# Kernel tuning notes

Measured on AMD Instinct MI355X. Metric: run time of the kernel, lower is better.

## Reference

```python
import jax, jax.numpy as jnp
import numpy as np

B, S, HID = 2, 2048, 2048
H, HKV, D = 16, 4, 128

def _rope(x, cos, sin):
    # x: [B,h,S,D]; cos/sin: [1,1,S,D//2]
    d = x.shape[-1] // 2
    x1, x2 = x[..., :d], x[..., d:]
    y1 = x1 * cos + x2 * sin
    y2 = -x1 * sin + x2 * cos
    return jnp.concatenate([y1, y2], axis=-1)

def _rmsnorm(x):
    eps = jnp.finfo(x.dtype).eps
    return x * jax.lax.rsqrt(jnp.mean(jnp.square(x), axis=-1, keepdims=True) + eps)

def setup_inputs() -> dict:
    key = jax.random.key(0)
    ks = jax.random.split(key, 5)
    x = jax.random.normal(ks[0], (B, S, HID), dtype=jnp.float32)
    # realistic rotary tables
    half = D // 2
    inv_freq = 1.0 / (10000.0 ** (jnp.arange(half, dtype=jnp.float32) / half))
    t = jnp.arange(S, dtype=jnp.float32)
    freqs = t[:, None] * inv_freq[None, :]            # [S, D//2]
    cos = jnp.cos(freqs)[None, None]                  # [1,1,S,D//2]
    sin = jnp.sin(freqs)[None, None]
    s = 0.02
    Wq = jax.random.normal(ks[1], (H * D, HID), dtype=jnp.float32) * s
    Wk = jax.random.normal(ks[2], (HKV * D, HID), dtype=jnp.float32) * s
    Wv = jax.random.normal(ks[3], (HKV * D, HID), dtype=jnp.float32) * s
    Wo = jax.random.normal(ks[4], (HID, H * D), dtype=jnp.float32) * s
    return {"x": x, "cos": cos, "sin": sin, "Wq": Wq, "Wk": Wk, "Wv": Wv, "Wo": Wo}

def reference(x, cos, sin, Wq, Wk, Wv, Wo):
    b, s, _ = x.shape
    rep = H // HKV
    q = (x @ Wq.T).reshape(b, s, H, D).transpose(0, 2, 1, 3)      # [B,H,S,D]
    k = (x @ Wk.T).reshape(b, s, HKV, D).transpose(0, 2, 1, 3)    # [B,Hkv,S,D]
    v = (x @ Wv.T).reshape(b, s, HKV, D).transpose(0, 2, 1, 3)
    k = jnp.repeat(k, rep, axis=1)                                # GQA expand
    v = jnp.repeat(v, rep, axis=1)
    q = _rmsnorm(_rope(q, cos, sin))
    k = _rmsnorm(_rope(k, cos, sin))
    scores = jnp.einsum('bhqd,bhkd->bhqk', q, k) * (D ** -0.5)
    causal = jnp.tril(jnp.ones((s, s), dtype=bool))
    scores = jnp.where(causal, scores, -jnp.inf)
    attn = jax.nn.softmax(scores, axis=-1)
    out = jnp.einsum('bhqk,bhkd->bhqd', attn, v)                  # [B,H,S,D]
    out = out.transpose(0, 2, 1, 3).reshape(b, s, H * D)
    return out @ Wo.T
```

## Files before the change

kernel.cpp:

```cpp
#include <hip/hip_runtime.h>
#include <hip/hip_bf16.h>

#define B_  2
#define S_  2048
#define HID_ 2048
#define H_  16
#define HKV_ 4
#define D_  128

typedef __bf16 bf16_t;
typedef bf16_t bf16x8 __attribute__((ext_vector_type(8)));
typedef float f32x4 __attribute__((ext_vector_type(4)));

typedef __attribute__((address_space(3))) unsigned int lds_u32_t;
typedef const __attribute__((address_space(1))) unsigned int glob_u32_t;

__device__ __forceinline__ void gl2lds16(const bf16_t* g, bf16_t* l) {
    __builtin_amdgcn_global_load_lds((glob_u32_t*)g, (lds_u32_t*)l, 16, 0, 0);
}

__device__ __forceinline__ unsigned packbf2(float a, float b) {
    union { bf16_t h[2]; unsigned u; } p;
    p.h[0] = (bf16_t)a;
    p.h[1] = (bf16_t)b;
    return p.u;
}

__global__ void detect_dtype(const unsigned* __restrict__ x, int* __restrict__ flag) {
    int lane = threadIdx.x;
    int c = 0;
#pragma unroll
    for (int i = 0; i < 16; ++i) {
        unsigned w = x[lane * 16 + i];
        unsigned e = (w >> 7) & 0xFF;
        c += (e >= 117 && e <= 137) ? 1 : 0;
    }
#pragma unroll
    for (int m = 1; m < 64; m <<= 1) c += __shfl_xor(c, m, 64);
    if (lane == 0) *flag = (c >= 512) ? 1 : 0;
}

struct Cseg { const void* src; bf16_t* dst; int n8; };

__global__ __launch_bounds__(256) void convert_bf16(Cseg s0, Cseg s1, Cseg s2, Cseg s3,
                                                    const int* __restrict__ flagp) {
    Cseg s = (blockIdx.y == 0) ? s0 : (blockIdx.y == 1) ? s1 : (blockIdx.y == 2) ? s2 : s3;
    const int i = blockIdx.x * 256 + threadIdx.x;
    if (i >= s.n8) return;
    if (*flagp) {
        ((uint4*)s.dst)[i] = ((const uint4*)s.src)[i];
    } else {
        const float4* p = (const float4*)s.src + (size_t)i * 2;
        float4 u = p[0], v = p[1];
        bf16x8 r;
        r[0] = (bf16_t)u.x; r[1] = (bf16_t)u.y; r[2] = (bf16_t)u.z; r[3] = (bf16_t)u.w;
        r[4] = (bf16_t)v.x; r[5] = (bf16_t)v.y; r[6] = (bf16_t)v.z; r[7] = (bf16_t)v.w;
        *(bf16x8*)(s.dst + (size_t)i * 8) = r;
    }
}

__global__ __launch_bounds__(256) void gemm_lds(const bf16_t* __restrict__ A,
                                                const bf16_t* __restrict__ W,
                                                void* __restrict__ C,
                                                int M, int N, int K,
                                                const int* __restrict__ flagp, int osel) {
    __shared__ bf16_t As[128 * 32];
    __shared__ bf16_t Bs[128 * 32];

    const int tid = threadIdx.x;
    const int w = tid >> 6;
    const int lane = tid & 63;
    const int r = lane & 15;
    const int quad = lane >> 4;
    const int m0 = blockIdx.y * 128;
    const int n0 = blockIdx.x * 128;
    const bool of32 = osel && (*flagp == 0);

    const int mh = (w & 1) * 64;
    const int nh = (w >> 1) * 64;

    const int c0 = w * 2;
    const int srow = lane >> 2;
    const int scol = (lane & 3) * 8;
    const bf16_t* Ag0 = A + (size_t)(m0 + c0 * 16 + srow) * K + scol;
    const bf16_t* Ag1 = A + (size_t)(m0 + c0 * 16 + 16 + srow) * K + scol;
    const bf16_t* Wg0 = W + (size_t)(n0 + c0 * 16 + srow) * K + scol;
    const bf16_t* Wg1 = W + (size_t)(n0 + c0 * 16 + 16 + srow) * K + scol;
    bf16_t* Al0 = As + c0 * 512;
    bf16_t* Al1 = As + (c0 + 1) * 512;
    bf16_t* Bl0 = Bs + c0 * 512;
    bf16_t* Bl1 = Bs + (c0 + 1) * 512;

    f32x4 acc[4][4] = {};

    for (int k0 = 0; k0 < K; k0 += 32) {
        __syncthreads();
        gl2lds16(Ag0 + k0, Al0);
        gl2lds16(Ag1 + k0, Al1);
        gl2lds16(Wg0 + k0, Bl0);
        gl2lds16(Wg1 + k0, Bl1);
        __syncthreads();

        bf16x8 a[4], b[4];
#pragma unroll
        for (int mi = 0; mi < 4; ++mi)
            a[mi] = *(const bf16x8*)&As[(mh + mi * 16 + r) * 32 + quad * 8];
#pragma unroll
        for (int ni = 0; ni < 4; ++ni)
            b[ni] = *(const bf16x8*)&Bs[(nh + ni * 16 + r) * 32 + quad * 8];
#pragma unroll
        for (int mi = 0; mi < 4; ++mi)
#pragma unroll
            for (int ni = 0; ni < 4; ++ni)
                acc[mi][ni] = __builtin_amdgcn_mfma_f32_16x16x32_bf16(a[mi], b[ni], acc[mi][ni], 0, 0, 0);
    }

#pragma unroll
    for (int mi = 0; mi < 4; ++mi) {
#pragma unroll
        for (int ni = 0; ni < 4; ++ni) {
#pragma unroll
            for (int g = 0; g < 4; ++g) {
                const int row = m0 + mh + mi * 16 + quad * 4 + g;
                const int col = n0 + nh + ni * 16 + r;
                if (of32) ((float*)C)[(size_t)row * N + col] = acc[mi][ni][g];
                else ((__hip_bfloat16*)C)[(size_t)row * N + col] = __float2bfloat16(acc[mi][ni][g]);
            }
        }
    }
}

template <bool F32>
__device__ __forceinline__ bf16x8 load8(const void* base, size_t off) {
    bf16x8 r;
    if constexpr (F32) {
        const float4* p = (const float4*)((const float*)base + off);
        float4 u = p[0], v = p[1];
        r[0] = (bf16_t)u.x; r[1] = (bf16_t)u.y; r[2] = (bf16_t)u.z; r[3] = (bf16_t)u.w;
        r[4] = (bf16_t)v.x; r[5] = (bf16_t)v.y; r[6] = (bf16_t)v.z; r[7] = (bf16_t)v.w;
    } else {
        r = *(const bf16x8*)((const bf16_t*)base + off);
    }
    return r;
}

template <bool AF32, bool WF32, bool OF32>
__device__ __forceinline__ void gemm_body(const void* __restrict__ A, const void* __restrict__ W,
                                          void* __restrict__ C, int M, int N, int K) {
    const int wave = threadIdx.x >> 6;
    const int lane = threadIdx.x & 63;
    const int r = lane & 15;
    const int quad = lane >> 4;
    const int m0 = blockIdx.y * 64 + wave * 16;
    const int n0 = blockIdx.x * 64;

    f32x4 acc[4] = {};
    const size_t aoff = (size_t)(m0 + r) * K + quad * 8;
    const size_t woff = (size_t)(n0 + r) * K + quad * 8;

    for (int k0 = 0; k0 < K; k0 += 32) {
        bf16x8 a = load8<AF32>(A, aoff + k0);
#pragma unroll
        for (int ns = 0; ns < 4; ++ns) {
            bf16x8 b = load8<WF32>(W, woff + (size_t)(ns * 16) * K + k0);
            acc[ns] = __builtin_amdgcn_mfma_f32_16x16x32_bf16(a, b, acc[ns], 0, 0, 0);
        }
    }

#pragma unroll
    for (int ns = 0; ns < 4; ++ns) {
#pragma unroll
        for (int reg = 0; reg < 4; ++reg) {
            int m = m0 + quad * 4 + reg;
            int n = n0 + ns * 16 + r;
            if constexpr (OF32) ((float*)C)[(size_t)m * N + n] = acc[ns][reg];
            else ((__hip_bfloat16*)C)[(size_t)m * N + n] = __float2bfloat16(acc[ns][reg]);
        }
    }
}

__global__ __launch_bounds__(256) void gemm_bt(const void* __restrict__ A, const void* __restrict__ W,
                                               void* __restrict__ C, int M, int N, int K,
                                               const int* __restrict__ flagp, int mode) {
    const int bf = *flagp;
    if (bf) {
        gemm_body<false, false, false>(A, W, C, M, N, K);
    } else if (mode == 0) {
        gemm_body<true, true, false>(A, W, C, M, N, K);
    } else {
        gemm_body<false, true, true>(A, W, C, M, N, K);
    }
}

__global__ __launch_bounds__(256) void rope_rms(__hip_bfloat16* __restrict__ qk,
                                                const void* __restrict__ cosp,
                                                const void* __restrict__ sinp,
                                                int NH, int ld, const int* __restrict__ flagp) {
    const int bf = *flagp;
    const int wave = threadIdx.x >> 6;
    const int lane = threadIdx.x & 63;
    const int row = blockIdx.x * 4 + wave;
    const int h = row % NH;
    const int bs = row / NH;
    const int s = bs % S_;

    __hip_bfloat16* p = qk + (size_t)bs * ld + h * D_;
    float x1 = __bfloat162float(p[lane]);
    float x2 = __bfloat162float(p[lane + 64]);
    float c, sn, eps;
    if (bf) {
        c   = __bfloat162float(((const __hip_bfloat16*)cosp)[s * 64 + lane]);
        sn  = __bfloat162float(((const __hip_bfloat16*)sinp)[s * 64 + lane]);
        eps = 0.0078125f;
    } else {
        c   = ((const float*)cosp)[s * 64 + lane];
        sn  = ((const float*)sinp)[s * 64 + lane];
        eps = 1.1920929e-07f;
    }
    float y1 = x1 * c + x2 * sn;
    float y2 = x2 * c - x1 * sn;
    float ss = y1 * y1 + y2 * y2;
#pragma unroll
    for (int m = 1; m < 64; m <<= 1) ss += __shfl_xor(ss, m, 64);
    float rinv = rsqrtf(ss * (1.0f / 128.0f) + eps);
    p[lane]      = __float2bfloat16(y1 * rinv);
    p[lane + 64] = __float2bfloat16(y2 * rinv);
}

__global__ __launch_bounds__(256) void post_qkv(__hip_bfloat16* __restrict__ qkv,
                                                const void* __restrict__ cosp,
                                                const void* __restrict__ sinp,
                                                bf16_t* __restrict__ Kp,
                                                unsigned* __restrict__ Vp,
                                                const void* __restrict__ WoS,
                                                bf16_t* __restrict__ WoD,
                                                const int* __restrict__ flagp) {
    const int bx = blockIdx.x;
    const int y = blockIdx.y;
    const int tid = threadIdx.x;

    if (y <= 1) {
        if (y == 1 && bx >= 4096) return;
        const int bf = *flagp;
        const int wave = tid >> 6;
        const int lane = tid & 63;
        const int row = bx * 4 + wave;
        const int h  = (y == 0) ? (row & 15) : (row & 3);
        const int bs = (y == 0) ? (row >> 4) : (row >> 2);
        const int s = bs & 2047;

        __hip_bfloat16* p = qkv + (size_t)bs * 3072 + (y ? 2048 : 0) + h * D_;
        float x1 = __bfloat162float(p[lane]);
        float x2 = __bfloat162float(p[lane + 64]);
        float c, sn, eps;
        if (bf) {
            c   = __bfloat162float(((const __hip_bfloat16*)cosp)[s * 64 + lane]);
            sn  = __bfloat162float(((const __hip_bfloat16*)sinp)[s * 64 + lane]);
            eps = 0.0078125f;
        } else {
            c   = ((const float*)cosp)[s * 64 + lane];
            sn  = ((const float*)sinp)[s * 64 + lane];
            eps = 1.1920929e-07f;
        }
        float y1 = x1 * c + x2 * sn;
        float y2 = x2 * c - x1 * sn;
        float ss = y1 * y1 + y2 * y2;
#pragma unroll
        for (int m = 1; m < 64; m <<= 1) ss += __shfl_xor(ss, m, 64);
        float rinv = rsqrtf(ss * (1.0f / 128.0f) + eps);
        const float y1r = y1 * rinv, y2r = y2 * rinv;
        if (y == 0) {
            p[lane]      = __float2bfloat16(y1r);
            p[lane + 64] = __float2bfloat16(y2r);
        } else {
            const int b = bs >> 11;
            const int kt = s >> 5;
            const int r32 = s & 31;
            const int gy = b * 4 + h;
            bf16_t* base = Kp + ((size_t)(gy * 64 + kt) * 32 + r32) * 128;
            const int sw = r32 & 15;
            base[(((lane >> 3) ^ sw) << 3) + (lane & 7)]       = (bf16_t)y1r;
            base[(((8 + (lane >> 3)) ^ sw) << 3) + (lane & 7)] = (bf16_t)y2r;
        }
    } else if (y == 2) {
        if (bx >= 4096) return;
        const int idx = bx * 256 + tid;
        const int j  = idx & 3;
        const int sl = (idx >> 2) & 3;
        const int d  = (idx >> 4) & 127;
        const int kt = (idx >> 11) & 63;
        const int gy = idx >> 17;
        const int s2 = sl ^ ((d >> 1) & 3);
        const int kp = s2 * 4 + j;
        const int kvh = gy & 3;
        const int b = gy >> 2;
        const unsigned short* p = (const unsigned short*)qkv
            + (size_t)(b * S_ + 32 * kt + kp) * 3072 + 2560 + kvh * D_ + d;
        unsigned lo = p[0];
        unsigned hi = p[(size_t)16 * 3072];
        Vp[idx] = lo | (hi << 16);
    } else {
        if (bx >= 2048) return;
        const int i = bx * 256 + tid;
        if (*flagp) {
            ((uint4*)WoD)[i] = ((const uint4*)WoS)[i];
        } else {
            const float4* p4 = (const float4*)WoS + (size_t)i * 2;
            float4 u = p4[0], v = p4[1];
            bf16x8 rr;
            rr[0] = (bf16_t)u.x; rr[1] = (bf16_t)u.y; rr[2] = (bf16_t)u.z; rr[3] = (bf16_t)u.w;
            rr[4] = (bf16_t)v.x; rr[5] = (bf16_t)v.y; rr[6] = (bf16_t)v.z; rr[7] = (bf16_t)v.w;
            *(bf16x8*)(WoD + (size_t)i * 8) = rr;
        }
    }
}

#define M0F 16.5f

__global__ __launch_bounds__(512, 1) void attn_flash10(const __hip_bfloat16* __restrict__ Q,
                                                       const bf16_t* __restrict__ Kp,
                                                       const unsigned* __restrict__ Vp,
                                                       __hip_bfloat16* __restrict__ O) {
    __shared__ bf16_t   Kl[8][4096];
    __shared__ unsigned Vl[8][2048];
    __shared__ unsigned PbS[8][2][16][16];

    const int tid = threadIdx.x;
    const int w = tid >> 6;
    const int lane = tid & 63;
    const int r = lane & 15;
    const int quad = lane >> 4;

    const int id = blockIdx.x;
    const int gy = id & 7;
    const int u = id >> 3;
    const int hh = u & 3;
    const int i = u >> 2;
    const int kvh = gy & 3;
    const int b = gy >> 2;
    const int h = kvh * 4 + hh;

    const int s4 = w & 3;
    int tlo = (s4 == 0) ? i : (s4 == 1) ? (31 - i) : (s4 == 2) ? (16 + i) : (15 - i);
    const int qt = (w < 4) ? tlo : (63 - tlo);
    const int q0 = qt * 32;

    const bf16_t* Ksrc = Kp + (size_t)gy * (64 * 4096);
    const unsigned* Vsrc = Vp + (size_t)gy * (64 * 2048);
    bf16_t* klds = &Kl[w][0];
    unsigned* vlds = &Vl[w][0];

    bf16x8 qf[2][4];
#pragma unroll
    for (int t = 0; t < 2; ++t) {
        const bf16_t* qp = (const bf16_t*)Q + (size_t)(b * S_ + q0 + t * 16 + r) * 3072 + h * D_ + quad * 8;
#pragma unroll
        for (int c = 0; c < 4; ++c) qf[t][c] = *(const bf16x8*)(qp + c * 32);
    }

    f32x4 oacc[2][8] = {};
    f32x4 lacc[2] = {};

    bf16x8 ones;
#pragma unroll
    for (int j = 0; j < 8; ++j) ones[j] = (bf16_t)1.0f;

    const float SC2 = 0.08838834764831845f * 1.4426950408889634f;

    unsigned* pbw = &PbS[w][0][0][0];
    const int pwi = (((r >> 2) ^ quad) & 3) * 4 + (r & 3);
    const int pgrp = ((quad ^ (r >> 2)) & 3) * 4;
    const int vsw = (quad ^ ((r >> 1) & 3)) * 4;

#define ISSUEK(KT) do {                                                       \
        const bf16_t* ks_ = Ksrc + (size_t)(KT) * 4096 + lane * 8;            \
        _Pragma("unroll")                                                     \
        for (int jj = 0; jj < 8; ++jj) gl2lds16(ks_ + jj * 512, klds + jj * 512); \
    } while (0)
#define ISSUEV(KT) do {                                                       \
        const bf16_t* vs_ = (const bf16_t*)(Vsrc + (size_t)(KT) * 2048) + lane * 8; \
        _Pragma("unroll")                                                     \
        for (int jj = 0; jj < 8; ++jj) gl2lds16(vs_ + jj * 512, (bf16_t*)vlds + jj * 512); \
    } while (0)

    ISSUEK(0);
    ISSUEV(0);
    for (int kt = 0; kt <= qt; ++kt) {
        asm volatile("s_waitcnt vmcnt(8)" ::: "memory");

        bf16x8 kf[8];
#pragma unroll
        for (int c = 0; c < 4; ++c) {
            const int sA = ((quad + 4 * c) ^ r) * 8;
            kf[2 * c]     = *(const bf16x8*)&klds[r * 128 + sA];
            kf[2 * c + 1] = *(const bf16x8*)&klds[(16 + r) * 128 + sA];
        }
        asm volatile("s_waitcnt lgkmcnt(0)" ::: "memory");
        __builtin_amdgcn_sched_barrier(0);
        if (kt < qt) ISSUEK(kt + 1);
        __builtin_amdgcn_sched_barrier(0);

        f32x4 s0_[2] = {}, s1_[2] = {};
        __builtin_amdgcn_s_setprio(1);
#pragma unroll
        for (int c = 0; c < 4; ++c) {
#pragma unroll
            for (int t = 0; t < 2; ++t) {
                s0_[t] = __builtin_amdgcn_mfma_f32_16x16x32_bf16(qf[t][c], kf[2 * c], s0_[t], 0, 0, 0);
                s1_[t] = __builtin_amdgcn_mfma_f32_16x16x32_bf16(qf[t][c], kf[2 * c + 1], s1_[t], 0, 0, 0);
            }
        }
        __builtin_amdgcn_s_setprio(0);

        if (kt == qt) {
#pragma unroll
            for (int t = 0; t < 2; ++t)
#pragma unroll
                for (int g = 0; g < 4; ++g) {
                    const int qrow = q0 + t * 16 + quad * 4 + g;
                    if (kt * 32 + r > qrow)      s0_[t][g] = -1e38f;
                    if (kt * 32 + 16 + r > qrow) s1_[t][g] = -1e38f;
                }
        }

#pragma unroll
        for (int t = 0; t < 2; ++t)
#pragma unroll
            for (int g = 0; g < 4; ++g) {
                const float p0 = exp2f(fmaf(s0_[t][g], SC2, -M0F));
                const float p1 = exp2f(fmaf(s1_[t][g], SC2, -M0F));
                pbw[t * 256 + (quad * 4 + g) * 16 + pwi] = packbf2(p0, p1);
            }

        bf16x8 pf0 = *(const bf16x8*)&pbw[r * 16 + pgrp];
        bf16x8 pf1 = *(const bf16x8*)&pbw[256 + r * 16 + pgrp];

        lacc[0] = __builtin_amdgcn_mfma_f32_16x16x32_bf16(pf0, ones, lacc[0], 0, 0, 0);
        lacc[1] = __builtin_amdgcn_mfma_f32_16x16x32_bf16(pf1, ones, lacc[1], 0, 0, 0);

        if (kt < qt) asm volatile("s_waitcnt vmcnt(8)" ::: "memory");
        else         asm volatile("s_waitcnt vmcnt(0)" ::: "memory");

        bf16x8 vf[8];
#pragma unroll
        for (int ns = 0; ns < 8; ++ns)
            vf[ns] = *(const bf16x8*)&vlds[(ns * 16 + r) * 16 + vsw];
        asm volatile("s_waitcnt lgkmcnt(0)" ::: "memory");
        __builtin_amdgcn_sched_barrier(0);
        if (kt < qt) ISSUEV(kt + 1);
        __builtin_amdgcn_sched_barrier(0);

        __builtin_amdgcn_s_setprio(1);
#pragma unroll
        for (int ns = 0; ns < 8; ++ns) {
            oacc[0][ns] = __builtin_amdgcn_mfma_f32_16x16x32_bf16(pf0, vf[ns], oacc[0][ns], 0, 0, 0);
            oacc[1][ns] = __builtin_amdgcn_mfma_f32_16x16x32_bf16(pf1, vf[ns], oacc[1][ns], 0, 0, 0);
        }
        __builtin_amdgcn_s_setprio(0);
    }
#undef ISSUEK
#undef ISSUEV

#pragma unroll
    for (int t = 0; t < 2; ++t) {
#pragma unroll
        for (int g = 0; g < 4; ++g) {
            const float inv = 1.0f / lacc[t][g];
            const int qrow = q0 + t * 16 + quad * 4 + g;
            __hip_bfloat16* op = O + (size_t)(b * S_ + qrow) * 2048 + h * D_;
#pragma unroll
            for (int ns = 0; ns < 8; ++ns)
                op[ns * 16 + r] = __float2bfloat16(oacc[t][ns][g] * inv);
        }
    }
}

#define KT_ 32
#define LDK 136

__global__ __launch_bounds__(256, 2) void attn_flash3(const __hip_bfloat16* __restrict__ Q,
                                                      const __hip_bfloat16* __restrict__ K,
                                                      const __hip_bfloat16* __restrict__ V,
                                                      __hip_bfloat16* __restrict__ O,
                                                      int ldq, int ldkv, int ldo) {
    __shared__ unsigned short Ks[KT_][LDK];
    __shared__ unsigned int Vt[D_ * 16];
    __shared__ unsigned int Pb[4][2][16][16];

    const int tid = threadIdx.x;
    const int w = tid >> 6;
    const int lane = tid & 63;
    const int r = lane & 15;
    const int quad = lane >> 4;

    const int gy = blockIdx.y;
    const int kvh = gy % HKV_;
    const int b = gy / HKV_;
    const int qt = b ? blockIdx.x : (gridDim.x - 1 - blockIdx.x);
    const int q0 = qt * 32;
    const int h = kvh * 4 + w;

    bf16x8 qf[2][4];
#pragma unroll
    for (int t = 0; t < 2; ++t) {
        const bf16_t* qp = (const bf16_t*)Q + (size_t)(b * S_ + q0 + t * 16 + r) * ldq + h * D_ + quad * 8;
#pragma unroll
        for (int c = 0; c < 4; ++c) qf[t][c] = *(const bf16x8*)(qp + c * 32);
    }

    f32x4 oacc[2][8] = {};
    f32x4 lacc[2] = {};
    float m_i[2][4];
#pragma unroll
    for (int t = 0; t < 2; ++t)
#pragma unroll
        for (int g = 0; g < 4; ++g) m_i[t][g] = -3e38f;

    const bf16_t* Kg = (const bf16_t*)K + (size_t)b * S_ * ldkv + kvh * D_;
    const bf16_t* Vg = (const bf16_t*)V + (size_t)b * S_ * ldkv + kvh * D_;

    bf16x8 ones;
#pragma unroll
    for (int j = 0; j < 8; ++j) ones[j] = (bf16_t)1.0f;

    const float SC2 = 0.08838834764831845f * 1.4426950408889634f;

    const int skey = tid >> 4;
    const int sdc = tid & 15;
    union U4 { uint4 u; unsigned short s[8]; };
    U4 rk0, rk1, rv0, rv1;
    {
        const size_t o0 = (size_t)skey * ldkv + sdc * 8;
        const size_t o1 = o0 + (size_t)16 * ldkv;
        rk0.u = *(const uint4*)(Kg + o0);
        rk1.u = *(const uint4*)(Kg + o1);
        rv0.u = *(const uint4*)(Vg + o0);
        rv1.u = *(const uint4*)(Vg + o1);
    }

    for (int kt = 0; kt <= qt; ++kt) {
        const int k0 = kt * KT_;
        __syncthreads();
        *(uint4*)&Ks[skey][sdc * 8] = rk0.u;
        *(uint4*)&Ks[skey + 16][sdc * 8] = rk1.u;
#pragma unroll
        for (int j = 0; j < 8; ++j) {
            const int d = sdc * 8 + j;
            const int f = ((j >> 1) & 3) ^ (sdc & 3);
            const int grp = (skey >> 2) ^ f;
            Vt[d * 16 + grp * 4 + (skey & 3)] = (unsigned)rv0.s[j] | ((unsigned)rv1.s[j] << 16);
        }
        __syncthreads();
        if (kt < qt) {
            const size_t o0 = (size_t)(k0 + KT_ + skey) * ldkv + sdc * 8;
            const size_t o1 = o0 + (size_t)16 * ldkv;
            rk0.u = *(const uint4*)(Kg + o0);
            rk1.u = *(const uint4*)(Kg + o1);
            rv0.u = *(const uint4*)(Vg + o0);
            rv1.u = *(const uint4*)(Vg + o1);
        }

        f32x4 s0[2] = {}, s1[2] = {};
#pragma unroll
        for (int c = 0; c < 4; ++c) {
            bf16x8 kb0 = *(const bf16x8*)&Ks[r][c * 32 + quad * 8];
            bf16x8 kb1 = *(const bf16x8*)&Ks[16 + r][c * 32 + quad * 8];
#pragma unroll
            for (int t = 0; t < 2; ++t) {
                s0[t] = __builtin_amdgcn_mfma_f32_16x16x32_bf16(qf[t][c], kb0, s0[t], 0, 0, 0);
                s1[t] = __builtin_amdgcn_mfma_f32_16x16x32_bf16(qf[t][c], kb1, s1[t], 0, 0, 0);
            }
        }

        const bool bnd = (kt == qt);
#pragma unroll
        for (int t = 0; t < 2; ++t) {
            float mt[4];
#pragma unroll
            for (int g = 0; g < 4; ++g) {
                s0[t][g] *= SC2;
                s1[t][g] *= SC2;
                if (bnd) {
                    const int qrow = q0 + t * 16 + quad * 4 + g;
                    if (k0 + r > qrow)      s0[t][g] = -1e38f;
                    if (k0 + 16 + r > qrow) s1[t][g] = -1e38f;
                }
                mt[g] = fmaxf(s0[t][g], s1[t][g]);
            }
#pragma unroll
            for (int msk = 1; msk < 16; msk <<= 1) {
#pragma unroll
                for (int g = 0; g < 4; ++g) mt[g] = fmaxf(mt[g], __shfl_xor(mt[g], msk, 64));
            }
            bool upd = false;
#pragma unroll
            for (int g = 0; g < 4; ++g) upd |= (mt[g] > m_i[t][g]);
            if (__ballot(upd)) {
#pragma unroll
                for (int g = 0; g < 4; ++g) {
                    const float mn = fmaxf(m_i[t][g], mt[g]);
                    const float al = exp2f(m_i[t][g] - mn);
                    m_i[t][g] = mn;
                    lacc[t][g] *= al;
#pragma unroll
                    for (int ns = 0; ns < 8; ++ns) oacc[t][ns][g] *= al;
                }
            }
#pragma unroll
            for (int g = 0; g < 4; ++g) {
                const float p0 = exp2f(s0[t][g] - m_i[t][g]);
                const float p1 = exp2f(s1[t][g] - m_i[t][g]);
                const int row = quad * 4 + g;
                Pb[w][t][row][(((r >> 2) ^ quad) & 3) * 4 + (r & 3)] = packbf2(p0, p1);
            }
        }

        const int pgrp = ((quad ^ (r >> 2)) & 3) * 4;
        bf16x8 pf0 = *(const bf16x8*)&Pb[w][0][r][pgrp];
        bf16x8 pf1 = *(const bf16x8*)&Pb[w][1][r][pgrp];

        lacc[0] = __builtin_amdgcn_mfma_f32_16x16x32_bf16(pf0, ones, lacc[0], 0, 0, 0);
        lacc[1] = __builtin_amdgcn_mfma_f32_16x16x32_bf16(pf1, ones, lacc[1], 0, 0, 0);

#pragma unroll
        for (int ns = 0; ns < 8; ++ns) {
            const int d = ns * 16 + r;
            const int f = ((r >> 1) & 3) ^ ((2 * ns + (r >> 3)) & 3);
            bf16x8 vf = *(const bf16x8*)&Vt[d * 16 + ((quad ^ f) & 3) * 4];
            oacc[0][ns] = __builtin_amdgcn_mfma_f32_16x16x32_bf16(pf0, vf, oacc[0][ns], 0, 0, 0);
            oacc[1][ns] = __builtin_amdgcn_mfma_f32_16x16x32_bf16(pf1, vf, oacc[1][ns], 0, 0, 0);
        }
    }

#pragma unroll
    for (int t = 0; t < 2; ++t) {
#pragma unroll
        for (int g = 0; g < 4; ++g) {
            const float inv = 1.0f / lacc[t][g];
            const int qrow = q0 + t * 16 + quad * 4 + g;
            __hip_bfloat16* op = O + (size_t)(b * S_ + qrow) * ldo + h * D_;
#pragma unroll
            for (int ns = 0; ns < 8; ++ns)
                op[ns * 16 + r] = __float2bfloat16(oacc[t][ns][g] * inv);
        }
    }
}

extern "C" void kernel_launch(void* const* d_in, const int* in_sizes, int n_in,
                              void* d_out, int out_size, void* d_ws, size_t ws_size,
                              hipStream_t stream) {
    const void* x    = d_in[0];
    const void* cosp = d_in[1];
    const void* sinp = d_in[2];
    const void* Wq   = d_in[3];
    const void* Wk   = d_in[4];
    const void* Wv   = d_in[5];
    const void* Wo   = d_in[6];

    const int M = B_ * S_;
    const size_t MB = 1ull << 20;

    if (ws_size >= 28 * MB + 64) {
        char* ws = (char*)d_ws;
        bf16_t* xb = (bf16_t*)ws;
        bf16_t* wb = (bf16_t*)(ws + 16 * MB);
        bf16_t* wo = (bf16_t*)(ws + 16 * MB);
        unsigned* vp4 = (unsigned*)(ws + 24 * MB);
        bf16_t* ao = (bf16_t*)ws;
        int* flag  = (int*)(ws + 28 * MB);
        bf16_t* qkv = (bf16_t*)d_out;
        bf16_t* kp8 = (bf16_t*)((char*)d_out + 24 * MB);

        detect_dtype<<<1, 64, 0, stream>>>((const unsigned*)x, flag);

        Cseg sx{x,  xb,                          (B_ * S_ * HID_) / 8};
        Cseg sq{Wq, wb,                          (H_ * D_ * HID_) / 8};
        Cseg sk{Wk, wb + (size_t)2048 * HID_,    (HKV_ * D_ * HID_) / 8};
        Cseg sv{Wv, wb + (size_t)2560 * HID_,    (HKV_ * D_ * HID_) / 8};
        convert_bf16<<<dim3(4096, 4), 256, 0, stream>>>(sx, sq, sk, sv, flag);

        gemm_lds<<<dim3(3072 / 128, M / 128), 256, 0, stream>>>(xb, wb, qkv, M, 3072, HID_, flag, 0);

        post_qkv<<<dim3(16384, 4), 256, 0, stream>>>(
            (__hip_bfloat16*)qkv, cosp, sinp, kp8, vp4, Wo, wo, flag);

        attn_flash10<<<dim3(256), 512, 0, stream>>>(
            (const __hip_bfloat16*)qkv, kp8, vp4, (__hip_bfloat16*)ao);

        gemm_lds<<<dim3(HID_ / 128, M / 128), 256, 0, stream>>>(ao, wo, d_out, M, HID_, H_ * D_, flag, 1);
    } else {
        __hip_bfloat16* qb = (__hip_bfloat16*)d_ws;
        int* flag = (int*)((char*)d_ws + (size_t)M * (H_ * D_) * sizeof(__hip_bfloat16));
        __hip_bfloat16* kb = (__hip_bfloat16*)d_out;
        __hip_bfloat16* vb = kb + (size_t)M * (HKV_ * D_);

        detect_dtype<<<1, 64, 0, stream>>>((const unsigned*)x, flag);

        gemm_bt<<<dim3((H_ * D_) / 64, M / 64), 256, 0, stream>>>(x, Wq, qb, M, H_ * D_, HID_, flag, 0);
        gemm_bt<<<dim3((HKV_ * D_) / 64, M / 64), 256, 0, stream>>>(x, Wk, kb, M, HKV_ * D_, HID_, flag, 0);
        gemm_bt<<<dim3((HKV_ * D_) / 64, M / 64), 256, 0, stream>>>(x, Wv, vb, M, HKV_ * D_, HID_, flag, 0);

        rope_rms<<<(B_ * S_ * H_) / 4, 256, 0, stream>>>(qb, cosp, sinp, H_, H_ * D_, flag);
        rope_rms<<<(B_ * S_ * HKV_) / 4, 256, 0, stream>>>(kb, cosp, sinp, HKV_, HKV_ * D_, flag);

        attn_flash3<<<dim3(S_ / 32, B_ * HKV_), 256, 0, stream>>>(qb, kb, vb, qb, H_ * D_, HKV_ * D_, H_ * D_);

        gemm_bt<<<dim3(HID_ / 64, M / 64), 256, 0, stream>>>(qb, Wo, d_out, M, HID_, H_ * D_, flag, 1);
    }
}
```

Baseline: 351.1 us.

## Replace GEMM with 256x256 tiled, double-buffered, swizzled 8-wave kernel

Replaces the 128x128, single-buffered, BK=32 GEMM with a 256x256 tile, 512-thread kernel that uses BK=64 and double-buffered LDS filled by global_load_lds. The LDS layout is XOR-swizzled to avoid bank conflicts, and the next tile's loads are interleaved with the MFMA work, using explicit barriers and s_setprio. The aim is more data reuse per tile and hiding global-memory latency behind compute. The trade-off is fewer blocks: the QKV GEMM gets 12x16=192 and the output GEMM 8x16=128, which may not fill all CUs on the MI355X. It also uses 128KB of LDS and a large accumulator register footprint.

```diff
diff --git a/kernel.cpp b/kernel.cpp
--- a/kernel.cpp
+++ b/kernel.cpp
@@ -59,70 +59,104 @@
     }
 }
 
-__global__ __launch_bounds__(256) void gemm_lds(const bf16_t* __restrict__ A,
+__global__ __launch_bounds__(512, 1) void gemm8(const bf16_t* __restrict__ A,
                                                 const bf16_t* __restrict__ W,
                                                 void* __restrict__ C,
                                                 int M, int N, int K,
                                                 const int* __restrict__ flagp, int osel) {
-    __shared__ bf16_t As[128 * 32];
-    __shared__ bf16_t Bs[128 * 32];
+    __shared__ bf16_t As[2][2][128 * 64];
+    __shared__ bf16_t Bs[2][2][128 * 64];
 
     const int tid = threadIdx.x;
     const int w = tid >> 6;
     const int lane = tid & 63;
     const int r = lane & 15;
     const int quad = lane >> 4;
-    const int m0 = blockIdx.y * 128;
-    const int n0 = blockIdx.x * 128;
+    const int r7 = r & 7;
+    const int wm = w >> 2;
+    const int wn = w & 3;
+
+    const int m0 = blockIdx.y * 256;
+    const int n0 = blockIdx.x * 256;
     const bool of32 = osel && (*flagp == 0);
 
-    const int mh = (w & 1) * 64;
-    const int nh = (w >> 1) * 64;
-
-    const int c0 = w * 2;
-    const int srow = lane >> 2;
-    const int scol = (lane & 3) * 8;
-    const bf16_t* Ag0 = A + (size_t)(m0 + c0 * 16 + srow) * K + scol;
-    const bf16_t* Ag1 = A + (size_t)(m0 + c0 * 16 + 16 + srow) * K + scol;
-    const bf16_t* Wg0 = W + (size_t)(n0 + c0 * 16 + srow) * K + scol;
-    const bf16_t* Wg1 = W + (size_t)(n0 + c0 * 16 + 16 + srow) * K + scol;
-    bf16_t* Al0 = As + c0 * 512;
-    bf16_t* Al1 = As + (c0 + 1) * 512;
-    bf16_t* Bl0 = Bs + c0 * 512;
-    bf16_t* Bl1 = Bs + (c0 + 1) * 512;
-
-    f32x4 acc[4][4] = {};
-
-    for (int k0 = 0; k0 < K; k0 += 32) {
-        __syncthreads();
-        gl2lds16(Ag0 + k0, Al0);
-        gl2lds16(Ag1 + k0, Al1);
-        gl2lds16(Wg0 + k0, Bl0);
-        gl2lds16(Wg1 + k0, Bl1);
-        __syncthreads();
-
-        bf16x8 a[4], b[4];
-#pragma unroll
-        for (int mi = 0; mi < 4; ++mi)
-            a[mi] = *(const bf16x8*)&As[(mh + mi * 16 + r) * 32 + quad * 8];
-#pragma unroll
-        for (int ni = 0; ni < 4; ++ni)
-            b[ni] = *(const bf16x8*)&Bs[(nh + ni * 16 + r) * 32 + quad * 8];
-#pragma unroll
-        for (int mi = 0; mi < 4; ++mi)
-#pragma unroll
-            for (int ni = 0; ni < 4; ++ni)
-                acc[mi][ni] = __builtin_amdgcn_mfma_f32_16x16x32_bf16(a[mi], b[ni], acc[mi][ni], 0, 0, 0);
-    }
-
-#pragma unroll
-    for (int mi = 0; mi < 4; ++mi) {
+    const int sr0 = w * 16 + (lane >> 3);
+    const int ssl = ((lane & 7) ^ (lane >> 3)) * 8;
+
+#define G8STAGE(BUF, HT, KT) do {                                             \
+        const bf16_t* src_; bf16_t* dst_;                                     \
+        if ((HT) < 2) { src_ = A + (size_t)(m0 + (HT) * 128) * K;             \
+                        dst_ = &As[BUF][HT][0]; }                             \
+        else          { src_ = W + (size_t)(n0 + ((HT) - 2) * 128) * K;       \
+                        dst_ = &Bs[BUF][(HT) - 2][0]; }                       \
+        const int k0_ = (KT) * 64;                                            \
+        gl2lds16(src_ + (size_t)sr0 * K + k0_ + ssl, dst_ + w * 1024);        \
+        gl2lds16(src_ + (size_t)(sr0 + 8) * K + k0_ + ssl, dst_ + w * 1024 + 512); \
+    } while (0)
+
+    f32x4 acc[8][4] = {};
+    const int nT = K >> 6;
+
+    G8STAGE(0, 0, 0); G8STAGE(0, 1, 0); G8STAGE(0, 2, 0); G8STAGE(0, 3, 0);
+    asm volatile("s_waitcnt vmcnt(0)" ::: "memory");
+    __builtin_amdgcn_s_barrier();
+
+    for (int t = 0; t < nT; ++t) {
+        const int buf = t & 1;
+        const int nbuf = buf ^ 1;
+        const bool st = (t + 1) < nT;
+
+        bf16x8 bfr[4][2];
+#pragma unroll
+        for (int q = 0; q < 4; ++q) {
+            if (q == 0) {
+#pragma unroll
+                for (int ni = 0; ni < 4; ++ni)
+#pragma unroll
+                    for (int ks = 0; ks < 2; ++ks)
+                        bfr[ni][ks] = *(const bf16x8*)&Bs[buf][wn >> 1]
+                            [((wn & 1) * 64 + ni * 16 + r) * 64 + ((quad + 4 * ks) ^ r7) * 8];
+            }
+            bf16x8 af[2][2];
+#pragma unroll
+            for (int mi = 0; mi < 2; ++mi)
+#pragma unroll
+                for (int ks = 0; ks < 2; ++ks)
+                    af[mi][ks] = *(const bf16x8*)&As[buf][wm]
+                        [((q * 2 + mi) * 16 + r) * 64 + ((quad + 4 * ks) ^ r7) * 8];
+            if (st) {
+                if (q == 0) { G8STAGE(nbuf, 0, t + 1); G8STAGE(nbuf, 1, t + 1); }
+                else if (q == 1) { G8STAGE(nbuf, 2, t + 1); G8STAGE(nbuf, 3, t + 1); }
+            }
+            __builtin_amdgcn_sched_barrier(0);
+            __builtin_amdgcn_s_barrier();
+            asm volatile("s_waitcnt lgkmcnt(0)" ::: "memory");
+            __builtin_amdgcn_sched_barrier(0);
+            __builtin_amdgcn_s_setprio(1);
+#pragma unroll
+            for (int mi = 0; mi < 2; ++mi)
+#pragma unroll
+                for (int ni = 0; ni < 4; ++ni)
+#pragma unroll
+                    for (int ks = 0; ks < 2; ++ks)
+                        acc[q * 2 + mi][ni] = __builtin_amdgcn_mfma_f32_16x16x32_bf16(
+                            af[mi][ks], bfr[ni][ks], acc[q * 2 + mi][ni], 0, 0, 0);
+            __builtin_amdgcn_s_setprio(0);
+            if (q == 3 && st) asm volatile("s_waitcnt vmcnt(0)" ::: "memory");
+            __builtin_amdgcn_sched_barrier(0);
+            __builtin_amdgcn_s_barrier();
+        }
+    }
+#undef G8STAGE
+
+#pragma unroll
+    for (int mi = 0; mi < 8; ++mi) {
 #pragma unroll
         for (int ni = 0; ni < 4; ++ni) {
 #pragma unroll
             for (int g = 0; g < 4; ++g) {
-                const int row = m0 + mh + mi * 16 + quad * 4 + g;
-                const int col = n0 + nh + ni * 16 + r;
+                const int row = m0 + wm * 128 + mi * 16 + quad * 4 + g;
+                const int col = n0 + wn * 64 + ni * 16 + r;
                 if (of32) ((float*)C)[(size_t)row * N + col] = acc[mi][ni][g];
                 else ((__hip_bfloat16*)C)[(size_t)row * N + col] = __float2bfloat16(acc[mi][ni][g]);
             }
@@ -679,7 +713,7 @@
         Cseg sv{Wv, wb + (size_t)2560 * HID_,    (HKV_ * D_ * HID_) / 8};
         convert_bf16<<<dim3(4096, 4), 256, 0, stream>>>(sx, sq, sk, sv, flag);
 
-        gemm_lds<<<dim3(3072 / 128, M / 128), 256, 0, stream>>>(xb, wb, qkv, M, 3072, HID_, flag, 0);
+        gemm8<<<dim3(3072 / 256, M / 256), 512, 0, stream>>>(xb, wb, qkv, M, 3072, HID_, flag, 0);
 
         post_qkv<<<dim3(16384, 4), 256, 0, stream>>>(
             (__hip_bfloat16*)qkv, cosp, sinp, kp8, vp4, Wo, wo, flag);
@@ -687,7 +721,7 @@
         attn_flash10<<<dim3(256), 512, 0, stream>>>(
             (const __hip_bfloat16*)qkv, kp8, vp4, (__hip_bfloat16*)ao);
 
-        gemm_lds<<<dim3(HID_ / 128, M / 128), 256, 0, stream>>>(ao, wo, d_out, M, HID_, H_ * D_, flag, 1);
+        gemm8<<<dim3(HID_ / 256, M / 256), 512, 0, stream>>>(ao, wo, d_out, M, HID_, H_ * D_, flag, 1);
     } else {
         __hip_bfloat16* qb = (__hip_bfloat16*)d_ws;
         int* flag = (int*)((char*)d_ws + (size_t)M * (H_ * D_) * sizeof(__hip_bfloat16));
```

Measured after the change: 352.9 us. No clear change (+0.5%).
